# Optimization experiments

Measured on AMD Instinct MI355X. Metric: run time of the kernel, lower is better.

Reference implementation:

```python
import jax, jax.numpy as jnp
import numpy as np

B, P, L, H = 64, 1024, 16, 256
NUM_SIZE = 18
TOPK = min(64, P)


def _ramp(epoch, a, b):
    if epoch <= a:
        return 0.0
    if epoch >= b:
        return 1.0
    return float(epoch - a) / float(b - a)


def _normalize(x):
    return x / jnp.maximum(jnp.linalg.norm(x, axis=-1, keepdims=True), 1e-12)


def setup_inputs() -> dict:
    key = jax.random.key(0)
    ks = jax.random.split(key, 16)
    return {
        'pred_center': jax.random.normal(ks[0], (B, P, 3), dtype=jnp.float32),
        'pred_size': jax.random.uniform(ks[1], (B, P, 3), minval=0.2, maxval=1.0, dtype=jnp.float32),
        'bbox_feature': jax.random.normal(ks[2], (B, P, H), dtype=jnp.float32),
        'objectness_scores': jax.random.normal(ks[3], (B, P, 2), dtype=jnp.float32),
        'lang_emb': jax.random.normal(ks[4], (B * L, H), dtype=jnp.float32),
        'lang_num': jax.random.randint(ks[5], (B,), 1, L + 1),
        'ref_center': jax.random.normal(ks[6], (B, L, 3), dtype=jnp.float32),
        'ref_size_class': jax.random.randint(ks[7], (B, L), 0, NUM_SIZE),
        'ref_size_residual': jax.random.uniform(ks[8], (B, L, 3), minval=0.0, maxval=0.2, dtype=jnp.float32),
        'mean_size_arr': jax.random.uniform(ks[9], (NUM_SIZE, 3), minval=0.3, maxval=1.5, dtype=jnp.float32),
        'W_text': jax.random.normal(ks[10], (H, H), dtype=jnp.float32) / np.sqrt(H),
        'W_pc': jax.random.normal(ks[11], (H, H), dtype=jnp.float32) / np.sqrt(H),
        'W_pc_iou': jax.random.normal(ks[12], (H, H), dtype=jnp.float32) / np.sqrt(H),
        'log_inv_tau': jnp.array([np.log(1.0 / 0.07)], dtype=jnp.float32),
        'epoch': 40,
    }


def _forward(pred_center, pred_size, bbox_feature, objectness_scores, lang_emb,
             lang_num, ref_center, ref_size_class, ref_size_residual,
             mean_size_arr, W_text, W_pc, W_pc_iou, log_inv_tau, epoch):
    b, l = ref_center.shape[:2]
    # curriculum (python scalars, epoch is a static int)
    p = _ramp(epoch, 0, 80)
    thr = 0.05 + 0.3 * p
    gamma = 1.0 + 2.0 * p
    min_tau = 0.08 - 0.04 * p

    # top-k proposals by objectness prob
    obj_prob = jax.nn.softmax(objectness_scores, axis=2)[..., 1]  # (B,P)
    _, topk_inds = jax.lax.top_k(obj_prob, TOPK)                  # (B,K)
    feat = jnp.take_along_axis(bbox_feature, topk_inds[..., None], axis=1)  # (B,K,H)
    ctr = jnp.take_along_axis(pred_center, topk_inds[..., None], axis=1)    # (B,K,3)
    sz = jnp.take_along_axis(pred_size, topk_inds[..., None], axis=1)       # (B,K,3)

    # axis-aligned 3D IoU between gt boxes (B,L) and pred boxes (B,K) -- detached
    gt_size = mean_size_arr[ref_size_class] + ref_size_residual + 0.01  # (B,L,3)
    gmin, gmax = ref_center - gt_size / 2, ref_center + gt_size / 2
    pmin, pmax = ctr - sz / 2, ctr + sz / 2
    lo = jnp.maximum(gmin[:, :, None], pmin[:, None])   # (B,L,K,3)
    hi = jnp.minimum(gmax[:, :, None], pmax[:, None])
    inter = jnp.prod(jnp.clip(hi - lo, 0.0, None), axis=-1)  # (B,L,K)
    vol_g = jnp.prod(gt_size, axis=-1)[:, :, None]
    vol_p = jnp.prod(sz, axis=-1)[:, None]
    iou = jax.lax.stop_gradient(inter / (vol_g + vol_p - inter + 1e-7))  # (B,L,K)

    # soft target over proposals (detached)
    w = jnp.clip(iou, 0.0, None) ** gamma * (iou >= thr).astype(iou.dtype)
    onehot = jax.nn.one_hot(jnp.argmax(iou, axis=-1), TOPK, dtype=iou.dtype)
    w = jnp.where(w.sum(-1, keepdims=True) < 1e-6, onehot, w)
    target = w / (w.sum(-1, keepdims=True) + 1e-6)  # (B,L,K)

    # temperature
    inv_tau = jnp.minimum(jnp.exp(log_inv_tau)[0], 100.0)
    inv_tau = jnp.minimum(inv_tau, 1.0 / max(min_tau, 1e-6))

    # language-box contrastive
    text = _normalize(lang_emb.reshape(b, l, -1) @ W_text.T)  # (B,L,H)
    boxf = _normalize(feat @ W_pc.T)                          # (B,K,H)
    sim = jnp.einsum('blh,bkh->blk', text, boxf)              # (B,L,K)
    logp = jax.nn.log_softmax(sim * inv_tau, axis=-1)
    t2 = target / (target.sum(-1, keepdims=True) + 1e-6)      # soft_ce renorm
    ce = -(t2 * logp).sum(-1)                                 # (B,L)

    neg = iou < 0.05
    s_neg = jnp.max(jnp.where(neg, sim, -jnp.inf), axis=-1)
    s_pos = (sim * target).sum(-1)
    rank = jnp.where(neg.any(-1), jax.nn.relu(0.2 - s_pos + s_neg), 0.0)
    lang_con = ce + 0.5 * rank                                # (B,L)

    mask = (jnp.arange(l)[None, :] < lang_num[:, None]).astype(sim.dtype)
    lang_loss = (lang_con * mask).sum() / b

    # iou-aware box-box contrastive
    tm = w[..., :, None] * w[..., None, :]                    # (B,L,K,K) detached
    tm = tm / (tm.sum(-1, keepdims=True) + 1e-6)
    tm = tm / (tm.sum(-1, keepdims=True) + 1e-6)              # soft_ce renorm
    boxf_iou = _normalize(feat @ W_pc_iou.T)                  # (B,K,H)
    sim_iou = jnp.einsum('bkh,bmh->bkm', boxf_iou, boxf_iou)  # (B,K,K)
    logp_iou = jax.nn.log_softmax(sim_iou * inv_tau, axis=-1)
    iou_ce = -(tm * logp_iou[:, None]).sum(-1).mean(-1)       # (B,L)
    iou_loss = (iou_ce * mask).sum() / b

    return jnp.stack([lang_loss, iou_loss])


def reference(pred_center, pred_size, bbox_feature, objectness_scores, lang_emb,
              lang_num, ref_center, ref_size_class, ref_size_residual,
              mean_size_arr, W_text, W_pc, W_pc_iou, log_inv_tau, epoch):
    return _forward(pred_center, pred_size, bbox_feature, objectness_scores,
                    lang_emb, lang_num, ref_center, ref_size_class,
                    ref_size_residual, mean_size_arr, W_text, W_pc, W_pc_iou,
                    log_inv_tau, epoch)
```

## Files before the change

kernel.cpp:

```cpp
#include <hip/hip_runtime.h>
#include <math.h>

#define B 64
#define P 1024
#define L 16
#define H 256
#define K 64

__device__ __forceinline__ float wsum(float v){
  #pragma unroll
  for (int o = 32; o >= 1; o >>= 1) v += __shfl_xor(v, o, 64);
  return v;
}
__device__ __forceinline__ float wmaxr(float v){
  #pragma unroll
  for (int o = 32; o >= 1; o >>= 1) v = fmaxf(v, __shfl_xor(v, o, 64));
  return v;
}
__device__ __forceinline__ void wargmax(float &v, int &i){
  #pragma unroll
  for (int o = 32; o >= 1; o >>= 1){
    float v2 = __shfl_xor(v, o, 64);
    int   i2 = __shfl_xor(i, o, 64);
    if (v2 > v || (v2 == v && i2 < i)){ v = v2; i = i2; }
  }
}
__device__ __forceinline__ unsigned fkey(float f){
  unsigned b = __float_as_uint(f);
  return (b & 0x80000000u) ? ~b : (b | 0x80000000u);
}
__device__ __forceinline__ float dot4(float4 a, float4 b){
  return a.x*b.x + a.y*b.y + a.z*b.z + a.w*b.w;
}
__device__ __forceinline__ int gsw(int r){ return (r ^ (r >> 3)) & 7; }

__global__ __launch_bounds__(256) void k_topk_iou(
    const float* __restrict__ pred_center, const float* __restrict__ pred_size,
    const float* __restrict__ obj, const float* __restrict__ ref_center,
    const int* __restrict__ ref_cls, const float* __restrict__ ref_res,
    const float* __restrict__ mean_sz, const int* __restrict__ epoch_p,
    const int* __restrict__ lang_num,
    int* __restrict__ inds, float* __restrict__ iou_ws, float* __restrict__ w_ws,
    float* __restrict__ c_ws)
{
  __shared__ int hist[256];
  __shared__ int s_digit, s_cum;
  __shared__ int waveTot[4];
  __shared__ int sel[K];
  __shared__ float ctrS[K][3], szS[K][3];
  int b = blockIdx.x, tid = threadIdx.x, lane = tid & 63, wave = tid >> 6;

  const float4* o4 = (const float4*)(obj + (size_t)b*P*2);
  float4 va = o4[tid*2], vb = o4[tid*2+1];
  unsigned kj[4] = { fkey(va.y - va.x), fkey(va.w - va.z),
                     fkey(vb.y - vb.x), fkey(vb.w - vb.z) };

  unsigned prefix = 0; int rem = K;
  for (int pass = 0; pass < 4; ++pass){
    int shift = 24 - pass*8;
    hist[tid] = 0;
    __syncthreads();
    #pragma unroll
    for (int j = 0; j < 4; ++j){
      unsigned kk = kj[j];
      bool cand = (pass == 0) || ((kk >> (shift + 8)) == prefix);
      if (cand) atomicAdd(&hist[(kk >> shift) & 0xff], 1);
    }
    __syncthreads();
    int d = 255 - tid;
    int h = hist[d];
    int s = h;
    #pragma unroll
    for (int o = 1; o < 64; o <<= 1){ int t = __shfl_up(s, o, 64); if (lane >= o) s += t; }
    if (lane == 63) waveTot[wave] = s;
    __syncthreads();
    #pragma unroll
    for (int q = 0; q < 3; ++q) if (q < wave) s += waveTot[q];
    if (s >= rem && s - h < rem){ s_digit = d; s_cum = s - h; }
    __syncthreads();
    prefix = (prefix << 8) | (unsigned)s_digit;
    rem -= s_cum;
    __syncthreads();
  }
  unsigned T = prefix;
  int remFinal = rem;

  int eqc = 0;
  #pragma unroll
  for (int j = 0; j < 4; ++j) eqc += (kj[j] == T) ? 1 : 0;
  int v = eqc;
  #pragma unroll
  for (int o = 1; o < 64; o <<= 1){ int t = __shfl_up(v, o, 64); if (lane >= o) v += t; }
  if (lane == 63) waveTot[wave] = v;
  __syncthreads();
  int off = 0;
  for (int q = 0; q < wave; ++q) off += waveTot[q];
  int e = off + v - eqc;
  __syncthreads();

  int selc = 0; bool ch[4];
  #pragma unroll
  for (int j = 0; j < 4; ++j){
    bool g = kj[j] > T;
    bool q = (kj[j] == T) && (e < remFinal);
    if (kj[j] == T) e++;
    ch[j] = g || q; selc += ch[j] ? 1 : 0;
  }
  v = selc;
  #pragma unroll
  for (int o = 1; o < 64; o <<= 1){ int t = __shfl_up(v, o, 64); if (lane >= o) v += t; }
  if (lane == 63) waveTot[wave] = v;
  __syncthreads();
  off = 0;
  for (int q = 0; q < wave; ++q) off += waveTot[q];
  int slot = off + v - selc;
  #pragma unroll
  for (int j = 0; j < 4; ++j) if (ch[j]) sel[slot++] = tid*4 + j;
  __syncthreads();

  if (tid < K){
    int idx = sel[tid];
    inds[b*K + tid] = idx;
    #pragma unroll
    for (int dd = 0; dd < 3; ++dd){
      ctrS[tid][dd] = pred_center[((size_t)b*P + idx)*3 + dd];
      szS [tid][dd] = pred_size [((size_t)b*P + idx)*3 + dd];
    }
  }
  __syncthreads();

  int ep = epoch_p[0];
  float pr = ep <= 0 ? 0.f : (ep >= 80 ? 1.f : ep / 80.f);
  float thr = 0.05f + 0.3f * pr;
  float gamma = 1.f + 2.f * pr;
  int ln = lang_num[b];

  for (int l = wave; l < L; l += 4){
    int cls = ref_cls[b*L + l];
    float gs[3], gc[3]; float volg = 1.f;
    #pragma unroll
    for (int dd = 0; dd < 3; ++dd){
      gs[dd] = mean_sz[cls*3+dd] + ref_res[((size_t)b*L+l)*3+dd] + 0.01f;
      gc[dd] = ref_center[((size_t)b*L+l)*3+dd];
      volg *= gs[dd];
    }
    int k = lane;
    float inter = 1.f, volp = 1.f;
    #pragma unroll
    for (int dd = 0; dd < 3; ++dd){
      float pc = ctrS[k][dd], ps = szS[k][dd];
      float lo = fmaxf(gc[dd]-gs[dd]*0.5f, pc-ps*0.5f);
      float hi = fminf(gc[dd]+gs[dd]*0.5f, pc+ps*0.5f);
      inter *= fmaxf(hi-lo, 0.f);
      volp *= ps;
    }
    float iou = inter / (volg + volp - inter + 1e-7f);
    float wv = (iou >= thr) ? powf(iou, gamma) : 0.f;
    float S = wsum(wv);
    float av = iou; int ai = k;
    wargmax(av, ai);
    float wfin = (S < 1e-6f) ? ((k == ai) ? 1.f : 0.f) : wv;
    iou_ws[((size_t)b*L + l)*K + k] = iou;
    w_ws  [((size_t)b*L + l)*K + k] = wfin;
    float Sf = (S < 1e-6f) ? 1.f : S;
    float a = wfin * Sf;
    float c = wfin / ((a + 1e-6f) * (a/(a + 1e-6f) + 1e-6f));
    c_ws[((size_t)b*L + l)*K + k] = (l < ln) ? c : 0.f;
  }
}

__global__ __launch_bounds__(256) void k_gemm(
    const float* __restrict__ bbox_feature, const int* __restrict__ inds,
    const float* __restrict__ lang_emb,
    const float* __restrict__ Wpc, const float* __restrict__ Wpci,
    const float* __restrict__ Wtext,
    float* __restrict__ boxr, float* __restrict__ boxri, float* __restrict__ texr)
{
  __shared__ float As[16][68], Ws[16][68];
  int gb = blockIdx.x;
  const float *W; float *C; int m0; bool gat;
  if (gb < 64)       { W = Wpc;   C = boxr;  m0 = gb*64;       gat = true;  }
  else if (gb < 128) { W = Wpci;  C = boxri; m0 = (gb-64)*64;  gat = true;  }
  else               { W = Wtext; C = texr;  m0 = (gb-128)*64; gat = false; }
  int bcol = blockIdx.y * 64;
  int tid = threadIdx.x;
  int lr = tid >> 2, lc = (tid & 3) * 4;
  int tr = tid >> 4, tc = tid & 15;
  int r = m0 + lr;
  const float* Arow = gat ? bbox_feature + ((size_t)(r >> 6)*P + inds[r])*H
                          : lang_emb + (size_t)r*H;
  const float* Wrow = W + (size_t)(bcol + lr)*H;
  float acc[4][4] = {};
  for (int h0 = 0; h0 < H; h0 += 16){
    float4 av = *(const float4*)&Arow[h0 + lc];
    float4 wv = *(const float4*)&Wrow[h0 + lc];
    As[lc+0][lr]=av.x; As[lc+1][lr]=av.y; As[lc+2][lr]=av.z; As[lc+3][lr]=av.w;
    Ws[lc+0][lr]=wv.x; Ws[lc+1][lr]=wv.y; Ws[lc+2][lr]=wv.z; Ws[lc+3][lr]=wv.w;
    __syncthreads();
    #pragma unroll
    for (int h = 0; h < 16; ++h){
      float4 a = *(const float4*)&As[h][tr*4];
      float4 w = *(const float4*)&Ws[h][tc*4];
      float aa[4] = {a.x,a.y,a.z,a.w};
      float ww[4] = {w.x,w.y,w.z,w.w};
      #pragma unroll
      for (int i = 0; i < 4; ++i)
        #pragma unroll
        for (int j = 0; j < 4; ++j) acc[i][j] += aa[i]*ww[j];
    }
    __syncthreads();
  }
  #pragma unroll
  for (int i = 0; i < 4; ++i){
    float4 v = make_float4(acc[i][0],acc[i][1],acc[i][2],acc[i][3]);
    *(float4*)&C[(size_t)(m0+tr*4+i)*H + bcol + tc*4] = v;
  }
}

__global__ __launch_bounds__(256) void k_contrast(
    const float* __restrict__ texr, const float* __restrict__ boxr,
    const float* __restrict__ boxri,
    const float* __restrict__ iou_ws, const float* __restrict__ w_ws,
    const float* __restrict__ c_ws,
    const int* __restrict__ lang_num, const float* __restrict__ log_inv_tau,
    const int* __restrict__ epoch_p, float* __restrict__ part)
{
  extern __shared__ __align__(16) float smem[];
  int tid = threadIdx.x, lane = tid & 63, wave = tid >> 6;
  int ep = epoch_p[0];
  float pr = ep <= 0 ? 0.f : (ep >= 80 ? 1.f : ep / 80.f);
  float min_tau = fmaxf(0.08f - 0.04f*pr, 1e-6f);
  float itau = fminf(fminf(expf(log_inv_tau[0]), 100.f), 1.f/min_tau);

  if (blockIdx.x < 64){
    int b = blockIdx.x;
    float4* TB = (float4*)smem;
    float4* TT = (float4*)smem + 4096;
    const float4* srcB = (const float4*)(boxr + (size_t)b*K*H);
    const float4* srcT = (const float4*)(texr + (size_t)b*L*H);
    #pragma unroll
    for (int j = 0; j < 16; ++j){
      int i4 = tid + 256*j;
      int row = i4 >> 6, c = i4 & 63;
      TB[row*64 + (c ^ gsw(row))] = srcB[i4];
    }
    #pragma unroll
    for (int j = 0; j < 4; ++j){
      int i4 = tid + 256*j;
      int row = i4 >> 6, c = i4 & 63;
      TT[row*64 + (c ^ gsw(row))] = srcT[i4];
    }
    __syncthreads();

    float acc[4] = {0,0,0,0}, nt2[4] = {0,0,0,0};
    float nb2 = 0.f;
    for (int c = 0; c < 64; ++c){
      float4 bx = TB[lane*64 + (c ^ gsw(lane))];
      nb2 += dot4(bx, bx);
      #pragma unroll
      for (int i = 0; i < 4; ++i){
        int l = wave*4 + i;
        float4 tv = TT[l*64 + (c ^ gsw(l))];
        acc[i] += dot4(tv, bx);
        nt2[i] += dot4(tv, tv);
      }
    }
    float nb = fmaxf(sqrtf(nb2), 1e-12f);
    int ln = lang_num[b];
    float bacc = 0.f;
    #pragma unroll
    for (int i = 0; i < 4; ++i){
      int l = wave*4 + i;
      if (l < ln){
        float sv = acc[i] / (fmaxf(sqrtf(nt2[i]), 1e-12f) * nb);
        float wv  = w_ws [((size_t)b*L + l)*K + lane];
        float iou = iou_ws[((size_t)b*L + l)*K + lane];
        float S2 = wsum(wv);
        float target = wv / (S2 + 1e-6f);
        float tsum = S2 / (S2 + 1e-6f);
        float t2 = target / (tsum + 1e-6f);
        float z = sv * itau;
        float zmax = wmaxr(z);
        float se = wsum(expf(z - zmax));
        float lp = z - zmax - logf(se);
        float ce = -wsum(t2 * lp);
        bool neg = iou < 0.05f;
        float sneg = wmaxr(neg ? sv : -INFINITY);
        int anyneg = __any(neg);
        float spos = wsum(sv * target);
        float rank = anyneg ? fmaxf(0.2f - spos + sneg, 0.f) : 0.f;
        bacc += ce + 0.5f*rank;
      }
    }
    if (lane == 0) part[blockIdx.x*4 + wave] = bacc;
  } else {
    int idx = blockIdx.x - 64;
    int b = idx >> 2, r0 = (idx & 3)*16 + wave*4;
    float4* TI = (float4*)smem;
    const float4* srcI = (const float4*)(boxri + (size_t)b*K*H);
    #pragma unroll
    for (int j = 0; j < 16; ++j){
      int i4 = tid + 256*j;
      int row = i4 >> 6, c = i4 & 63;
      TI[row*64 + (c ^ gsw(row))] = srcI[i4];
    }
    float wl[16];
    #pragma unroll
    for (int l = 0; l < 16; ++l) wl[l] = w_ws[((size_t)b*L + l)*K + lane];
    __syncthreads();

    float acc[4] = {0,0,0,0};
    float nm2 = 0.f;
    for (int c = 0; c < 64; ++c){
      float4 bx = TI[lane*64 + (c ^ gsw(lane))];
      nm2 += dot4(bx, bx);
      #pragma unroll
      for (int i = 0; i < 4; ++i){
        float4 kq = TI[(r0+i)*64 + (c ^ gsw(r0+i))];
        acc[i] += dot4(kq, bx);
      }
    }
    float nm = fmaxf(sqrtf(nm2), 1e-12f);
    float contrib = 0.f;
    #pragma unroll
    for (int i = 0; i < 4; ++i){
      float nk = __shfl(nm, r0 + i, 64);
      float sv = acc[i] / (nk * nm);
      float z = sv * itau;
      float zmax = wmaxr(z);
      float se = wsum(expf(z - zmax));
      float lp = z - zmax - logf(se);
      float M = 0.f;
      #pragma unroll
      for (int l = 0; l < 16; ++l)
        M += c_ws[((size_t)b*L + l)*K + (r0 + i)] * wl[l];
      contrib += M * lp;
    }
    float bacc = -wsum(contrib) * (1.f/64.f);
    if (lane == 0) part[256 + idx*4 + wave] = bacc;
  }
}

__global__ __launch_bounds__(256) void k_final(const float* __restrict__ part,
                                               float* __restrict__ out)
{
  __shared__ float redI[4], redL[4];
  int tid = threadIdx.x, lane = tid & 63, wave = tid >> 6;
  float vl = part[tid];
  float vi = part[256+tid] + part[512+tid] + part[768+tid] + part[1024+tid];
  vi = wsum(vi);
  vl = wsum(vl);
  if (lane == 0){ redI[wave] = vi; redL[wave] = vl; }
  __syncthreads();
  if (tid == 0){
    out[0] = (redL[0]+redL[1]+redL[2]+redL[3]) * (1.f/64.f);
    out[1] = (redI[0]+redI[1]+redI[2]+redI[3]) * (1.f/64.f);
  }
}

extern "C" void kernel_launch(void* const* d_in, const int* in_sizes, int n_in,
                              void* d_out, int out_size, void* d_ws, size_t ws_size,
                              hipStream_t stream)
{
  const float* pred_center = (const float*)d_in[0];
  const float* pred_size   = (const float*)d_in[1];
  const float* bbox_feature= (const float*)d_in[2];
  const float* obj         = (const float*)d_in[3];
  const float* lang_emb    = (const float*)d_in[4];
  const int*   lang_num    = (const int*)d_in[5];
  const float* ref_center  = (const float*)d_in[6];
  const int*   ref_cls     = (const int*)d_in[7];
  const float* ref_res     = (const float*)d_in[8];
  const float* mean_sz     = (const float*)d_in[9];
  const float* Wtext       = (const float*)d_in[10];
  const float* Wpc         = (const float*)d_in[11];
  const float* Wpci        = (const float*)d_in[12];
  const float* lit         = (const float*)d_in[13];
  const int*   epoch       = (const int*)d_in[14];

  float* ws = (float*)d_ws;
  int*   inds   = (int*)ws;
  float* iou_ws = ws + 4096;
  float* w_ws   = iou_ws + B*L*K;
  float* c_ws   = w_ws + B*L*K;
  float* texr   = c_ws + B*L*K;
  float* boxr   = texr + (size_t)B*L*H;
  float* boxri  = boxr + (size_t)B*K*H;
  float* part   = boxri + (size_t)B*K*H;

  k_topk_iou<<<B, 256, 0, stream>>>(pred_center, pred_size, obj, ref_center,
                                    ref_cls, ref_res, mean_sz, epoch, lang_num,
                                    inds, iou_ws, w_ws, c_ws);
  k_gemm<<<dim3(144, 4), 256, 0, stream>>>(bbox_feature, inds, lang_emb,
                                           Wpc, Wpci, Wtext, boxr, boxri, texr);
  k_contrast<<<320, 256, 81920, stream>>>(texr, boxr, boxri,
                                          iou_ws, w_ws, c_ws, lang_num, lit,
                                          epoch, part);
  k_final<<<1, 256, 0, stream>>>(part, (float*)d_out);
}
```

Measured before the change: 61.58 us.

## Store GEMM outputs in column-chunk-major layout and read directly in contrast kernel

The GEMM kernel now writes its projected features in a layout where consecutive rows are contiguous for each float4 column chunk. This lets the contrast kernel read from global memory with coalesced loads instead of staging 64-80KB into swizzled LDS. Removing the LDS staging, the barrier and the large dynamic shared allocation should raise occupancy and cut the copy cost. In exchange, the repeated broadcast reads of text and query rows now come from L1/L2 rather than LDS, and the GEMM stores become more strided.

Result: slower. 88.74 us (+44.1%).

```diff
diff --git a/kernel.cpp b/kernel.cpp
--- a/kernel.cpp
+++ b/kernel.cpp
@@ -32,7 +32,6 @@
 __device__ __forceinline__ float dot4(float4 a, float4 b){
   return a.x*b.x + a.y*b.y + a.z*b.z + a.w*b.w;
 }
-__device__ __forceinline__ int gsw(int r){ return (r ^ (r >> 3)) & 7; }
 
 __global__ __launch_bounds__(256) void k_topk_iou(
     const float* __restrict__ pred_center, const float* __restrict__ pred_size,
@@ -174,14 +173,14 @@
     const float* __restrict__ lang_emb,
     const float* __restrict__ Wpc, const float* __restrict__ Wpci,
     const float* __restrict__ Wtext,
-    float* __restrict__ boxr, float* __restrict__ boxri, float* __restrict__ texr)
+    float* __restrict__ cboxr, float* __restrict__ cboxri, float* __restrict__ ctexr)
 {
   __shared__ float As[16][68], Ws[16][68];
   int gb = blockIdx.x;
   const float *W; float *C; int m0; bool gat;
-  if (gb < 64)       { W = Wpc;   C = boxr;  m0 = gb*64;       gat = true;  }
-  else if (gb < 128) { W = Wpci;  C = boxri; m0 = (gb-64)*64;  gat = true;  }
-  else               { W = Wtext; C = texr;  m0 = (gb-128)*64; gat = false; }
+  if (gb < 64)       { W = Wpc;   C = cboxr;  m0 = gb*64;       gat = true;  }
+  else if (gb < 128) { W = Wpci;  C = cboxri; m0 = (gb-64)*64;  gat = true;  }
+  else               { W = Wtext; C = ctexr;  m0 = (gb-128)*64; gat = false; }
   int bcol = blockIdx.y * 64;
   int tid = threadIdx.x;
   int lr = tid >> 2, lc = (tid & 3) * 4;
@@ -210,22 +209,29 @@
     }
     __syncthreads();
   }
+  int hg = (bcol >> 2) + tc;
   #pragma unroll
   for (int i = 0; i < 4; ++i){
     float4 v = make_float4(acc[i][0],acc[i][1],acc[i][2],acc[i][3]);
-    *(float4*)&C[(size_t)(m0+tr*4+i)*H + bcol + tc*4] = v;
+    int rr = m0 + tr*4 + i;
+    if (gat){
+      int bb = rr >> 6, rl = rr & 63;
+      *(float4*)&C[(size_t)bb*16384 + hg*256 + rl*4] = v;
+    } else {
+      int bb = rr >> 4, rl = rr & 15;
+      *(float4*)&C[(size_t)bb*4096  + hg*64  + rl*4] = v;
+    }
   }
 }
 
 __global__ __launch_bounds__(256) void k_contrast(
-    const float* __restrict__ texr, const float* __restrict__ boxr,
-    const float* __restrict__ boxri,
+    const float* __restrict__ ctexr, const float* __restrict__ cboxr,
+    const float* __restrict__ cboxri,
     const float* __restrict__ iou_ws, const float* __restrict__ w_ws,
     const float* __restrict__ c_ws,
     const int* __restrict__ lang_num, const float* __restrict__ log_inv_tau,
     const int* __restrict__ epoch_p, float* __restrict__ part)
 {
-  extern __shared__ __align__(16) float smem[];
   int tid = threadIdx.x, lane = tid & 63, wave = tid >> 6;
   int ep = epoch_p[0];
   float pr = ep <= 0 ? 0.f : (ep >= 80 ? 1.f : ep / 80.f);
@@ -234,33 +240,18 @@
 
   if (blockIdx.x < 64){
     int b = blockIdx.x;
-    float4* TB = (float4*)smem;
-    float4* TT = (float4*)smem + 4096;
-    const float4* srcB = (const float4*)(boxr + (size_t)b*K*H);
-    const float4* srcT = (const float4*)(texr + (size_t)b*L*H);
-    #pragma unroll
-    for (int j = 0; j < 16; ++j){
-      int i4 = tid + 256*j;
-      int row = i4 >> 6, c = i4 & 63;
-      TB[row*64 + (c ^ gsw(row))] = srcB[i4];
-    }
-    #pragma unroll
-    for (int j = 0; j < 4; ++j){
-      int i4 = tid + 256*j;
-      int row = i4 >> 6, c = i4 & 63;
-      TT[row*64 + (c ^ gsw(row))] = srcT[i4];
-    }
-    __syncthreads();
-
+    const float4* TB = (const float4*)cboxr + (size_t)b*4096;
+    const float4* TT = (const float4*)ctexr + (size_t)b*1024;
+    int l0 = wave*4;
     float acc[4] = {0,0,0,0}, nt2[4] = {0,0,0,0};
     float nb2 = 0.f;
+    #pragma unroll 4
     for (int c = 0; c < 64; ++c){
-      float4 bx = TB[lane*64 + (c ^ gsw(lane))];
+      float4 bx = TB[c*64 + lane];
       nb2 += dot4(bx, bx);
       #pragma unroll
       for (int i = 0; i < 4; ++i){
-        int l = wave*4 + i;
-        float4 tv = TT[l*64 + (c ^ gsw(l))];
+        float4 tv = TT[c*16 + l0 + i];
         acc[i] += dot4(tv, bx);
         nt2[i] += dot4(tv, tv);
       }
@@ -270,7 +261,7 @@
     float bacc = 0.f;
     #pragma unroll
     for (int i = 0; i < 4; ++i){
-      int l = wave*4 + i;
+      int l = l0 + i;
       if (l < ln){
         float sv = acc[i] / (fmaxf(sqrtf(nt2[i]), 1e-12f) * nb);
         float wv  = w_ws [((size_t)b*L + l)*K + lane];
@@ -296,27 +287,19 @@
   } else {
     int idx = blockIdx.x - 64;
     int b = idx >> 2, r0 = (idx & 3)*16 + wave*4;
-    float4* TI = (float4*)smem;
-    const float4* srcI = (const float4*)(boxri + (size_t)b*K*H);
-    #pragma unroll
-    for (int j = 0; j < 16; ++j){
-      int i4 = tid + 256*j;
-      int row = i4 >> 6, c = i4 & 63;
-      TI[row*64 + (c ^ gsw(row))] = srcI[i4];
-    }
+    const float4* TI = (const float4*)cboxri + (size_t)b*4096;
     float wl[16];
     #pragma unroll
     for (int l = 0; l < 16; ++l) wl[l] = w_ws[((size_t)b*L + l)*K + lane];
-    __syncthreads();
-
     float acc[4] = {0,0,0,0};
     float nm2 = 0.f;
+    #pragma unroll 4
     for (int c = 0; c < 64; ++c){
-      float4 bx = TI[lane*64 + (c ^ gsw(lane))];
+      float4 bx = TI[c*64 + lane];
       nm2 += dot4(bx, bx);
       #pragma unroll
       for (int i = 0; i < 4; ++i){
-        float4 kq = TI[(r0+i)*64 + (c ^ gsw(r0+i))];
+        float4 kq = TI[c*64 + r0 + i];
         acc[i] += dot4(kq, bx);
       }
     }
@@ -383,18 +366,18 @@
   float* iou_ws = ws + 4096;
   float* w_ws   = iou_ws + B*L*K;
   float* c_ws   = w_ws + B*L*K;
-  float* texr   = c_ws + B*L*K;
-  float* boxr   = texr + (size_t)B*L*H;
-  float* boxri  = boxr + (size_t)B*K*H;
-  float* part   = boxri + (size_t)B*K*H;
+  float* ctexr  = c_ws + B*L*K;
+  float* cboxr  = ctexr + (size_t)B*L*H;
+  float* cboxri = cboxr + (size_t)B*K*H;
+  float* part   = cboxri + (size_t)B*K*H;
 
   k_topk_iou<<<B, 256, 0, stream>>>(pred_center, pred_size, obj, ref_center,
                                     ref_cls, ref_res, mean_sz, epoch, lang_num,
                                     inds, iou_ws, w_ws, c_ws);
   k_gemm<<<dim3(144, 4), 256, 0, stream>>>(bbox_feature, inds, lang_emb,
-                                           Wpc, Wpci, Wtext, boxr, boxri, texr);
-  k_contrast<<<320, 256, 81920, stream>>>(texr, boxr, boxri,
-                                          iou_ws, w_ws, c_ws, lang_num, lit,
-                                          epoch, part);
+                                           Wpc, Wpci, Wtext, cboxr, cboxri, ctexr);
+  k_contrast<<<320, 256, 0, stream>>>(ctexr, cboxr, cboxri,
+                                      iou_ws, w_ws, c_ws, lang_num, lit,
+                                      epoch, part);
   k_final<<<1, 256, 0, stream>>>(part, (float*)d_out);
 }
```
